# Kernel optimization log

Hardware: AMD Instinct MI355X
Metric: run time of the kernel (lower is better)

Reference implementation:

```python
import jax, jax.numpy as jnp
import numpy as np

B, D_IN, D_HID, D_OUT, E = 8192, 1024, 4096, 1024, 8


def setup_inputs() -> dict:
    key = jax.random.key(0)
    ks = jax.random.split(key, 6)
    s_in = 1.0 / np.sqrt(D_IN)
    s_gh = 1.0 / np.sqrt(D_HID // 2)
    s_eh = 1.0 / np.sqrt(D_HID)
    return {
        "x": jax.random.normal(ks[0], (B, D_IN), jnp.float32),
        "gW1": jax.random.normal(ks[1], (D_IN, D_HID // 2), jnp.float32) * s_in,
        "gb1": jnp.zeros((D_HID // 2,), jnp.float32),
        "gW2": jax.random.normal(ks[2], (D_HID // 2, E), jnp.float32) * s_gh,
        "gb2": jnp.zeros((E,), jnp.float32),
        "eW1": jax.random.normal(ks[3], (E, D_IN, D_HID), jnp.float32) * s_in,
        "eb1": jnp.zeros((E, D_HID), jnp.float32),
        "eW2": jax.random.normal(ks[4], (E, D_HID, D_OUT), jnp.float32) * s_eh,
        "eb2": jnp.zeros((E, D_OUT), jnp.float32),
    }


def reference(x, gW1, gb1, gW2, gb2, eW1, eb1, eW2, eb2):
    # Gating network: Linear -> ReLU -> (Dropout: eval identity) -> Linear -> Softmax(dim=1)
    gh = jax.nn.relu(x @ gW1 + gb1)                      # [B, H/2]
    gates = jax.nn.softmax(gh @ gW2 + gb2, axis=1)       # [B, E]

    # All experts run on the full batch (dense MoE): batched GEMMs over expert axis.
    h = jax.nn.relu(jnp.einsum('bi,eih->beh', x, eW1) + eb1)   # [B, E, H]
    eo = jnp.einsum('beh,eho->beo', h, eW2) + eb2              # [B, E, O]

    # Gated weighted sum over experts.
    combined = jnp.einsum('beo,be->bo', eo, gates)             # [B, O]
    return (combined, gates, gates)
```

## Files before the change

### kernel.cpp

```cpp
#include <hip/hip_runtime.h>
#include <hip/hip_bf16.h>
#include <stdint.h>

#define BB 8192
#define DIN 1024
#define DHID 4096
#define DOUT 1024
#define NEXP 8
#define GH_N 2048

typedef __attribute__((ext_vector_type(8))) __bf16 bf16x8;
typedef __attribute__((ext_vector_type(4))) float f32x4;

__device__ inline unsigned short f2bf(float f) {
  unsigned u = __builtin_bit_cast(unsigned, f);
  u = (u + 0x7FFFu + ((u >> 16) & 1u)) >> 16;
  return (unsigned short)u;
}
__device__ inline float b2f(unsigned short s) {
  return __builtin_bit_cast(float, (unsigned)s << 16);
}

__global__ void cvt_f32_bf16(const float* __restrict__ in,
                             unsigned short* __restrict__ out, int n4) {
  int i = blockIdx.x * blockDim.x + threadIdx.x;
  if (i >= n4) return;
  float4 v = ((const float4*)in)[i];
  ushort4 o;
  o.x = f2bf(v.x); o.y = f2bf(v.y); o.z = f2bf(v.z); o.w = f2bf(v.w);
  ((ushort4*)out)[i] = o;
}

__global__ void transpose_cvt(const float* __restrict__ in,
                              unsigned short* __restrict__ out, int R, int C) {
  __shared__ float tile[32][33];
  int c0 = blockIdx.x * 32, r0 = blockIdx.y * 32;
  int tx = threadIdx.x & 31, ty = threadIdx.x >> 5;
#pragma unroll
  for (int i = 0; i < 4; ++i)
    tile[ty + i * 8][tx] = in[(size_t)(r0 + ty + i * 8) * C + c0 + tx];
  __syncthreads();
#pragma unroll
  for (int i = 0; i < 4; ++i)
    out[(size_t)(c0 + ty + i * 8) * R + r0 + tx] = f2bf(tile[tx][ty + i * 8]);
}

__device__ inline void gload16(const void* g, void* l) {
  __builtin_amdgcn_global_load_lds(
      (const __attribute__((address_space(1))) void*)g,
      (__attribute__((address_space(3))) void*)l, 16, 0, 0);
}

template <int N>
__device__ inline void waitv() {
  if constexpr (N == 0) asm volatile("s_waitcnt vmcnt(0)" ::: "memory");
  else if constexpr (N == 2) asm volatile("s_waitcnt vmcnt(2)" ::: "memory");
  else asm volatile("s_waitcnt vmcnt(0)" ::: "memory");
}
__device__ inline void waitlgkm0() {
  asm volatile("s_waitcnt lgkmcnt(0)" ::: "memory");
  __builtin_amdgcn_sched_barrier(0);
}

template <int EPI>
__global__ __launch_bounds__(512, 4)
void gemmO(const unsigned short* __restrict__ A,
           const unsigned short* __restrict__ Bt,
           int M, int N, int K,
           const float* __restrict__ bias,
           unsigned short* __restrict__ outb,
           float* __restrict__ outf,
           const float* __restrict__ gates,
           int eidx, int accum) {
  constexpr int BK = 32;
  constexpr int TSZ = 128 * BK;
  __shared__ unsigned short As[3 * TSZ];
  __shared__ unsigned short Bs[3 * TSZ];

  const int t = threadIdx.x;
  const int lane = t & 63;
  const int wid = t >> 6;
  const int wm = wid >> 1;
  const int wn = wid & 1;

  const int nwg = gridDim.x;
  const int flat = blockIdx.x;
  const int swz = (flat & 7) * (nwg >> 3) + (flat >> 3);
  const int nbn = N >> 7;
  const int bn = swz % nbn, bm = swz / nbn;
  const int m0 = bm << 7, n0 = bn << 7;

  const int row = t >> 2, cp = t & 3;
  const int c = cp ^ ((row >> 1) & 3);
  const unsigned short* aS = A + (size_t)(m0 + row) * K + c * 8;
  const unsigned short* bS = Bt + (size_t)(n0 + row) * K + c * 8;
  const int qoff = t * 8;

  auto stage = [&](int T) {
    const int b = T % 3;
    const int k0 = T * BK;
    gload16(aS + k0, As + b * TSZ + qoff);
    gload16(bS + k0, Bs + b * TSZ + qoff);
  };

  const int l15 = lane & 15, lg = lane >> 4;
  int aoff[2], boff[4];
#pragma unroll
  for (int mi = 0; mi < 2; ++mi) {
    int r = wm * 32 + mi * 16 + l15;
    aoff[mi] = r * BK + ((lg ^ ((r >> 1) & 3)) << 3);
  }
#pragma unroll
  for (int ni = 0; ni < 4; ++ni) {
    int r = wn * 64 + ni * 16 + l15;
    boff[ni] = r * BK + ((lg ^ ((r >> 1) & 3)) << 3);
  }

  f32x4 acc[2][4];
  const f32x4 zero = {0.f, 0.f, 0.f, 0.f};
#pragma unroll
  for (int mi = 0; mi < 2; ++mi)
#pragma unroll
    for (int ni = 0; ni < 4; ++ni) acc[mi][ni] = zero;

  const int NT = K >> 5;

  stage(0);
  stage(1);
  waitv<2>();
  __builtin_amdgcn_s_barrier();

  for (int T = 0; T < NT; ++T) {
    const int b = T % 3;
    const unsigned short* Ab = As + b * TSZ;
    const unsigned short* Bb = Bs + b * TSZ;
    bf16x8 af[2], bfr[4];
#pragma unroll
    for (int mi = 0; mi < 2; ++mi) af[mi] = *(const bf16x8*)(Ab + aoff[mi]);
#pragma unroll
    for (int ni = 0; ni < 4; ++ni) bfr[ni] = *(const bf16x8*)(Bb + boff[ni]);
    if (T + 2 < NT) stage(T + 2);
    waitlgkm0();
    __builtin_amdgcn_s_setprio(1);
#pragma unroll
    for (int mi = 0; mi < 2; ++mi)
#pragma unroll
      for (int ni = 0; ni < 4; ++ni)
        acc[mi][ni] = __builtin_amdgcn_mfma_f32_16x16x32_bf16(
            af[mi], bfr[ni], acc[mi][ni], 0, 0, 0);
    __builtin_amdgcn_s_setprio(0);
    __builtin_amdgcn_sched_barrier(0);
    if (T + 2 < NT) waitv<2>();
    else if (T + 1 < NT) waitv<0>();
    __builtin_amdgcn_s_barrier();
  }

  const int rb = m0 + wm * 32 + (lg << 2);
  const int cb = n0 + wn * 64 + l15;
  if (EPI == 0) {
#pragma unroll
    for (int mi = 0; mi < 2; ++mi) {
#pragma unroll
      for (int ni = 0; ni < 4; ++ni) {
        int col = cb + ni * 16;
        float bv = bias[col];
#pragma unroll
        for (int r = 0; r < 4; ++r) {
          int rowo = rb + mi * 16 + r;
          float v = acc[mi][ni][r] + bv;
          outb[(size_t)rowo * N + col] = f2bf(fmaxf(v, 0.f));
        }
      }
    }
  } else {
#pragma unroll
    for (int mi = 0; mi < 2; ++mi) {
      float g[4];
#pragma unroll
      for (int r = 0; r < 4; ++r)
        g[r] = gates[(size_t)(rb + mi * 16 + r) * NEXP + eidx];
#pragma unroll
      for (int ni = 0; ni < 4; ++ni) {
        int col = cb + ni * 16;
        float bv = bias[col];
#pragma unroll
        for (int r = 0; r < 4; ++r) {
          size_t o = (size_t)(rb + mi * 16 + r) * N + col;
          float v = (acc[mi][ni][r] + bv) * g[r];
          outf[o] = accum ? outf[o] + v : v;
        }
      }
    }
  }
}

__global__ void gating_head(const unsigned short* __restrict__ gh,
                            const float* __restrict__ gW2,
                            const float* __restrict__ gb2,
                            float* __restrict__ gws,
                            float* __restrict__ g1,
                            float* __restrict__ g2, int B, int Kh) {
  int gw = (blockIdx.x * blockDim.x + threadIdx.x) >> 6;
  int lane = threadIdx.x & 63;
  int nw = (gridDim.x * blockDim.x) >> 6;
  for (int row = gw; row < B; row += nw) {
    float s[8] = {0, 0, 0, 0, 0, 0, 0, 0};
    for (int k = lane; k < Kh; k += 64) {
      float hv = b2f(gh[(size_t)row * Kh + k]);
      const float* w = gW2 + (size_t)k * 8;
#pragma unroll
      for (int e = 0; e < 8; ++e) s[e] += hv * w[e];
    }
#pragma unroll
    for (int e = 0; e < 8; ++e) {
#pragma unroll
      for (int off = 32; off > 0; off >>= 1) s[e] += __shfl_xor(s[e], off, 64);
    }
    if (lane == 0) {
      float l[8], m = -1e30f;
#pragma unroll
      for (int e = 0; e < 8; ++e) {
        l[e] = s[e] + gb2[e];
        m = fmaxf(m, l[e]);
      }
      float sum = 0.f;
#pragma unroll
      for (int e = 0; e < 8; ++e) {
        l[e] = expf(l[e] - m);
        sum += l[e];
      }
      float inv = 1.f / sum;
#pragma unroll
      for (int e = 0; e < 8; ++e) {
        float gv = l[e] * inv;
        gws[(size_t)row * 8 + e] = gv;
        g1[(size_t)row * 8 + e] = gv;
        g2[(size_t)row * 8 + e] = gv;
      }
    }
  }
}

extern "C" void kernel_launch(void* const* d_in, const int* in_sizes, int n_in,
                              void* d_out, int out_size, void* d_ws,
                              size_t ws_size, hipStream_t stream) {
  (void)in_sizes; (void)n_in; (void)out_size; (void)ws_size;
  const float* x   = (const float*)d_in[0];
  const float* gW1 = (const float*)d_in[1];
  const float* gb1 = (const float*)d_in[2];
  const float* gW2 = (const float*)d_in[3];
  const float* gb2 = (const float*)d_in[4];
  const float* eW1 = (const float*)d_in[5];
  const float* eb1 = (const float*)d_in[6];
  const float* eW2 = (const float*)d_in[7];
  const float* eb2 = (const float*)d_in[8];

  float* outC  = (float*)d_out;
  float* outG1 = outC + (size_t)BB * DOUT;
  float* outG2 = outG1 + (size_t)BB * NEXP;

  char* ws = (char*)d_ws;
  unsigned short* xb   = (unsigned short*)(ws);
  unsigned short* gW1T = (unsigned short*)(ws + 16777216);
  unsigned short* gh   = (unsigned short*)(ws + 20971520);
  float*          gat  = (float*)(ws + 54525952);
  unsigned short* w1T  = (unsigned short*)(ws + 54788096);
  unsigned short* w2T  = (unsigned short*)(ws + 63176704);
  unsigned short* hbuf = (unsigned short*)(ws + 71565312);

  cvt_f32_bf16<<<(BB * DIN / 4) / 256, 256, 0, stream>>>(x, xb, BB * DIN / 4);
  transpose_cvt<<<dim3(GH_N / 32, DIN / 32), 256, 0, stream>>>(gW1, gW1T, DIN, GH_N);
  gemmO<0><<<dim3((BB / 128) * (GH_N / 128)), 512, 0, stream>>>(
      xb, gW1T, BB, GH_N, DIN, gb1, gh, nullptr, nullptr, 0, 0);
  gating_head<<<256, 256, 0, stream>>>(gh, gW2, gb2, gat, outG1, outG2, BB, GH_N);

  for (int e = 0; e < NEXP; ++e) {
    transpose_cvt<<<dim3(DHID / 32, DIN / 32), 256, 0, stream>>>(
        eW1 + (size_t)e * DIN * DHID, w1T, DIN, DHID);
    transpose_cvt<<<dim3(DOUT / 32, DHID / 32), 256, 0, stream>>>(
        eW2 + (size_t)e * DHID * DOUT, w2T, DHID, DOUT);
    gemmO<0><<<dim3((BB / 128) * (DHID / 128)), 512, 0, stream>>>(
        xb, w1T, BB, DHID, DIN, eb1 + (size_t)e * DHID, hbuf, nullptr, nullptr, 0, 0);
    gemmO<1><<<dim3((BB / 128) * (DOUT / 128)), 512, 0, stream>>>(
        hbuf, w2T, BB, DOUT, DHID, eb2 + (size_t)e * DOUT, nullptr, outC, gat, e, e > 0);
  }
}
```

Before: 1.622 ms.

## Use larger 256-wide GEMM tiles with double-buffered quarter-phase pipeline; rewrite gating head

The 128x128 triple-buffered GEMM is replaced by a templated kernel using 256x256 tiles (or 128x256 for the second expert GEMM) with BK=64 and double buffering. Each K step is split into four MFMA phases, interleaving LDS fragment reads and async global-to-LDS loads between barriers. The aim is higher arithmetic intensity per LDS/global byte and better latency hiding, at the cost of fewer resident workgroups and many more barriers. The gating head is also rewritten to stage gW2 transposed in LDS, use vectorized loads, and assign one wave per row.

```diff
diff --git a/kernel.cpp b/kernel.cpp
--- a/kernel.cpp
+++ b/kernel.cpp
@@ -54,17 +54,21 @@
 template <int N>
 __device__ inline void waitv() {
   if constexpr (N == 0) asm volatile("s_waitcnt vmcnt(0)" ::: "memory");
+  else if constexpr (N == 1) asm volatile("s_waitcnt vmcnt(1)" ::: "memory");
   else if constexpr (N == 2) asm volatile("s_waitcnt vmcnt(2)" ::: "memory");
+  else if constexpr (N == 3) asm volatile("s_waitcnt vmcnt(3)" ::: "memory");
+  else if constexpr (N == 4) asm volatile("s_waitcnt vmcnt(4)" ::: "memory");
   else asm volatile("s_waitcnt vmcnt(0)" ::: "memory");
 }
 __device__ inline void waitlgkm0() {
   asm volatile("s_waitcnt lgkmcnt(0)" ::: "memory");
   __builtin_amdgcn_sched_barrier(0);
 }
-
-template <int EPI>
-__global__ __launch_bounds__(512, 4)
-void gemmO(const unsigned short* __restrict__ A,
+__device__ inline bf16x8 ldr(const char* p) { return *(const bf16x8*)p; }
+
+template <int BM, int EPI>
+__global__ __launch_bounds__(512, 2)
+void gemmP(const unsigned short* __restrict__ A,
            const unsigned short* __restrict__ Bt,
            int M, int N, int K,
            const float* __restrict__ bias,
@@ -72,121 +76,228 @@
            float* __restrict__ outf,
            const float* __restrict__ gates,
            int eidx, int accum) {
-  constexpr int BK = 32;
-  constexpr int TSZ = 128 * BK;
-  __shared__ unsigned short As[3 * TSZ];
-  __shared__ unsigned short Bs[3 * TSZ];
+  constexpr int BN = 256;
+  constexpr int WROWS = BM / 2;
+  constexpr int RM = WROWS / 16;
+  constexpr int HM = RM / 2;
+  constexpr int ABYTES = BM * 128;
+  constexpr int BBYTES = BN * 128;
+  constexpr int AUN = BM / 64;
+  constexpr int WS = (BM == 256) ? 4 : 3;
+  constexpr int W0L = (BM == 256) ? 2 : 1;
+
+  __shared__ char lds[2 * (ABYTES + BBYTES)];
+  char* Als = lds;
+  char* Bls = lds + 2 * ABYTES;
 
   const int t = threadIdx.x;
   const int lane = t & 63;
   const int wid = t >> 6;
-  const int wm = wid >> 1;
-  const int wn = wid & 1;
-
-  const int nwg = gridDim.x;
-  const int flat = blockIdx.x;
+  const int wm = wid >> 2;
+  const int wn = wid & 3;
+  const int l15 = lane & 15, lg = lane >> 4;
+
+  const int nwg = gridDim.x, flat = blockIdx.x;
   const int swz = (flat & 7) * (nwg >> 3) + (flat >> 3);
-  const int nbn = N >> 7;
+  const int nbn = N >> 8;
   const int bn = swz % nbn, bm = swz / nbn;
-  const int m0 = bm << 7, n0 = bn << 7;
-
-  const int row = t >> 2, cp = t & 3;
-  const int c = cp ^ ((row >> 1) & 3);
-  const unsigned short* aS = A + (size_t)(m0 + row) * K + c * 8;
-  const unsigned short* bS = Bt + (size_t)(n0 + row) * K + c * 8;
-  const int qoff = t * 8;
-
-  auto stage = [&](int T) {
-    const int b = T % 3;
-    const int k0 = T * BK;
-    gload16(aS + k0, As + b * TSZ + qoff);
-    gload16(bS + k0, Bs + b * TSZ + qoff);
-  };
-
-  const int l15 = lane & 15, lg = lane >> 4;
-  int aoff[2], boff[4];
-#pragma unroll
-  for (int mi = 0; mi < 2; ++mi) {
-    int r = wm * 32 + mi * 16 + l15;
-    aoff[mi] = r * BK + ((lg ^ ((r >> 1) & 3)) << 3);
-  }
-#pragma unroll
-  for (int ni = 0; ni < 4; ++ni) {
-    int r = wn * 64 + ni * 16 + l15;
-    boff[ni] = r * BK + ((lg ^ ((r >> 1) & 3)) << 3);
-  }
-
-  f32x4 acc[2][4];
+  const int m0 = bm * BM, n0 = bn * BN;
+
+  const int prow = t >> 3;
+  const int cOff = ((t & 7) ^ (prow & 7)) * 8;
+  const unsigned short* aP[AUN];
+  const unsigned short* bP[4];
+#pragma unroll
+  for (int u = 0; u < AUN; ++u) {
+    int p = u * 64 + prow;
+    int g;
+    if (BM == 256) g = ((p >> 6) & 1) * 128 + ((p >> 7) & 1) * 64 + (p & 63);
+    else           g = ((p >> 5) & 1) * 64  + ((p >> 6) & 1) * 32 + (p & 31);
+    aP[u] = A + (size_t)(m0 + g) * K + cOff;
+  }
+#pragma unroll
+  for (int u = 0; u < 4; ++u) {
+    int p = u * 64 + prow;
+    int g = ((p >> 5) & 3) * 64 + ((p >> 7) & 1) * 32 + (p & 31);
+    bP[u] = Bt + (size_t)(n0 + g) * K + cOff;
+  }
+  const int ldst = t * 16;
+
+  const int slot0 = ((lg) ^ (l15 & 7)) * 16;
+  const int slot1 = ((4 + lg) ^ (l15 & 7)) * 16;
+  const int aRB0 = (0 * (BM / 2) + wm * (WROWS / 2) + l15) * 128;
+  const int aRB1 = (1 * (BM / 2) + wm * (WROWS / 2) + l15) * 128;
+  const int bCB0 = (0 * (BN / 2) + wn * 32 + l15) * 128;
+  const int bCB1 = (1 * (BN / 2) + wn * 32 + l15) * 128;
+
+  f32x4 acc[RM][4];
   const f32x4 zero = {0.f, 0.f, 0.f, 0.f};
 #pragma unroll
-  for (int mi = 0; mi < 2; ++mi)
-#pragma unroll
-    for (int ni = 0; ni < 4; ++ni) acc[mi][ni] = zero;
-
-  const int NT = K >> 5;
-
-  stage(0);
-  stage(1);
-  waitv<2>();
+  for (int i = 0; i < RM; ++i)
+#pragma unroll
+    for (int j = 0; j < 4; ++j) acc[i][j] = zero;
+
+  bf16x8 ar[HM][2], bc0[2][2], bc1[2][2];
+
+  const int NT = K >> 6;
+
+  {
+    gload16(bP[0], Bls + 0 * 8192 + ldst);
+    gload16(bP[1], Bls + 1 * 8192 + ldst);
+    gload16(aP[0], Als + 0 * 8192 + ldst);
+    if (AUN == 4) gload16(aP[1], Als + 1 * 8192 + ldst);
+    gload16(bP[2], Bls + 2 * 8192 + ldst);
+    gload16(bP[3], Bls + 3 * 8192 + ldst);
+    if (AUN == 4) {
+      gload16(aP[2], Als + 2 * 8192 + ldst);
+      gload16(aP[3], Als + 3 * 8192 + ldst);
+    } else {
+      gload16(aP[1], Als + 1 * 8192 + ldst);
+    }
+  }
+  waitv<WS>();
   __builtin_amdgcn_s_barrier();
 
   for (int T = 0; T < NT; ++T) {
-    const int b = T % 3;
-    const unsigned short* Ab = As + b * TSZ;
-    const unsigned short* Bb = Bs + b * TSZ;
-    bf16x8 af[2], bfr[4];
-#pragma unroll
-    for (int mi = 0; mi < 2; ++mi) af[mi] = *(const bf16x8*)(Ab + aoff[mi]);
-#pragma unroll
-    for (int ni = 0; ni < 4; ++ni) bfr[ni] = *(const bf16x8*)(Bb + boff[ni]);
-    if (T + 2 < NT) stage(T + 2);
+    const int buf = T & 1;
+    const char* Ab = Als + buf * ABYTES;
+    const char* Bb = Bls + buf * BBYTES;
+    char* An = Als + (buf ^ 1) * ABYTES;
+    char* Bn = Bls + (buf ^ 1) * BBYTES;
+    const bool stg = (T + 1 < NT);
+    const int kn = (T + 1) << 6;
+
+#pragma unroll
+    for (int f = 0; f < HM; ++f) {
+      ar[f][0] = ldr(Ab + aRB0 + f * 2048 + slot0);
+      ar[f][1] = ldr(Ab + aRB0 + f * 2048 + slot1);
+    }
+#pragma unroll
+    for (int c = 0; c < 2; ++c) {
+      bc0[c][0] = ldr(Bb + bCB0 + c * 2048 + slot0);
+      bc0[c][1] = ldr(Bb + bCB0 + c * 2048 + slot1);
+    }
+    if (stg) {
+      gload16(bP[0] + kn, Bn + 0 * 8192 + ldst);
+      gload16(bP[1] + kn, Bn + 1 * 8192 + ldst);
+    }
+    __builtin_amdgcn_s_barrier();
     waitlgkm0();
     __builtin_amdgcn_s_setprio(1);
 #pragma unroll
-    for (int mi = 0; mi < 2; ++mi)
-#pragma unroll
-      for (int ni = 0; ni < 4; ++ni)
-        acc[mi][ni] = __builtin_amdgcn_mfma_f32_16x16x32_bf16(
-            af[mi], bfr[ni], acc[mi][ni], 0, 0, 0);
+    for (int ks = 0; ks < 2; ++ks)
+#pragma unroll
+      for (int f = 0; f < HM; ++f)
+#pragma unroll
+        for (int c = 0; c < 2; ++c)
+          acc[f][c] = __builtin_amdgcn_mfma_f32_16x16x32_bf16(
+              ar[f][ks], bc0[c][ks], acc[f][c], 0, 0, 0);
     __builtin_amdgcn_s_setprio(0);
-    __builtin_amdgcn_sched_barrier(0);
-    if (T + 2 < NT) waitv<2>();
-    else if (T + 1 < NT) waitv<0>();
-    __builtin_amdgcn_s_barrier();
-  }
-
-  const int rb = m0 + wm * 32 + (lg << 2);
+    if (stg) waitv<WS>(); else waitv<W0L>();
+    __builtin_amdgcn_s_barrier();
+
+#pragma unroll
+    for (int c = 0; c < 2; ++c) {
+      bc1[c][0] = ldr(Bb + bCB1 + c * 2048 + slot0);
+      bc1[c][1] = ldr(Bb + bCB1 + c * 2048 + slot1);
+    }
+    if (stg) {
+      gload16(aP[0] + kn, An + 0 * 8192 + ldst);
+      if (AUN == 4) gload16(aP[1] + kn, An + 1 * 8192 + ldst);
+    }
+    __builtin_amdgcn_s_barrier();
+    waitlgkm0();
+    __builtin_amdgcn_s_setprio(1);
+#pragma unroll
+    for (int ks = 0; ks < 2; ++ks)
+#pragma unroll
+      for (int f = 0; f < HM; ++f)
+#pragma unroll
+        for (int c = 0; c < 2; ++c)
+          acc[f][2 + c] = __builtin_amdgcn_mfma_f32_16x16x32_bf16(
+              ar[f][ks], bc1[c][ks], acc[f][2 + c], 0, 0, 0);
+    __builtin_amdgcn_s_setprio(0);
+    if (stg) waitv<WS>(); else waitv<0>();
+    __builtin_amdgcn_s_barrier();
+
+#pragma unroll
+    for (int f = 0; f < HM; ++f) {
+      ar[f][0] = ldr(Ab + aRB1 + f * 2048 + slot0);
+      ar[f][1] = ldr(Ab + aRB1 + f * 2048 + slot1);
+    }
+    if (stg) {
+      gload16(bP[2] + kn, Bn + 2 * 8192 + ldst);
+      gload16(bP[3] + kn, Bn + 3 * 8192 + ldst);
+    }
+    __builtin_amdgcn_s_barrier();
+    waitlgkm0();
+    __builtin_amdgcn_s_setprio(1);
+#pragma unroll
+    for (int ks = 0; ks < 2; ++ks)
+#pragma unroll
+      for (int f = 0; f < HM; ++f)
+#pragma unroll
+        for (int c = 0; c < 2; ++c)
+          acc[HM + f][2 + c] = __builtin_amdgcn_mfma_f32_16x16x32_bf16(
+              ar[f][ks], bc1[c][ks], acc[HM + f][2 + c], 0, 0, 0);
+    __builtin_amdgcn_s_setprio(0);
+    __builtin_amdgcn_s_barrier();
+
+    if (stg) {
+      if (AUN == 4) {
+        gload16(aP[2] + kn, An + 2 * 8192 + ldst);
+        gload16(aP[3] + kn, An + 3 * 8192 + ldst);
+      } else {
+        gload16(aP[1] + kn, An + 1 * 8192 + ldst);
+      }
+    }
+    __builtin_amdgcn_s_barrier();
+    __builtin_amdgcn_s_setprio(1);
+#pragma unroll
+    for (int ks = 0; ks < 2; ++ks)
+#pragma unroll
+      for (int f = 0; f < HM; ++f)
+#pragma unroll
+        for (int c = 0; c < 2; ++c)
+          acc[HM + f][c] = __builtin_amdgcn_mfma_f32_16x16x32_bf16(
+              ar[f][ks], bc0[c][ks], acc[HM + f][c], 0, 0, 0);
+    __builtin_amdgcn_s_setprio(0);
+    if (stg) waitv<WS>();
+    __builtin_amdgcn_s_barrier();
+  }
+
+  const int rb = m0 + wm * WROWS + (lg << 2);
   const int cb = n0 + wn * 64 + l15;
   if (EPI == 0) {
 #pragma unroll
-    for (int mi = 0; mi < 2; ++mi) {
-#pragma unroll
-      for (int ni = 0; ni < 4; ++ni) {
-        int col = cb + ni * 16;
+    for (int fg = 0; fg < RM; ++fg) {
+#pragma unroll
+      for (int j = 0; j < 4; ++j) {
+        int col = cb + j * 16;
         float bv = bias[col];
 #pragma unroll
         for (int r = 0; r < 4; ++r) {
-          int rowo = rb + mi * 16 + r;
-          float v = acc[mi][ni][r] + bv;
-          outb[(size_t)rowo * N + col] = f2bf(fmaxf(v, 0.f));
+          int row = rb + fg * 16 + r;
+          float v = acc[fg][j][r] + bv;
+          outb[(size_t)row * N + col] = f2bf(fmaxf(v, 0.f));
         }
       }
     }
   } else {
 #pragma unroll
-    for (int mi = 0; mi < 2; ++mi) {
+    for (int fg = 0; fg < RM; ++fg) {
       float g[4];
 #pragma unroll
       for (int r = 0; r < 4; ++r)
-        g[r] = gates[(size_t)(rb + mi * 16 + r) * NEXP + eidx];
-#pragma unroll
-      for (int ni = 0; ni < 4; ++ni) {
-        int col = cb + ni * 16;
+        g[r] = gates[(size_t)(rb + fg * 16 + r) * NEXP + eidx];
+#pragma unroll
+      for (int j = 0; j < 4; ++j) {
+        int col = cb + j * 16;
         float bv = bias[col];
 #pragma unroll
         for (int r = 0; r < 4; ++r) {
-          size_t o = (size_t)(rb + mi * 16 + r) * N + col;
-          float v = (acc[mi][ni][r] + bv) * g[r];
+          size_t o = (size_t)(rb + fg * 16 + r) * N + col;
+          float v = (acc[fg][j][r] + bv) * g[r];
           outf[o] = accum ? outf[o] + v : v;
         }
       }
@@ -194,49 +305,58 @@
   }
 }
 
-__global__ void gating_head(const unsigned short* __restrict__ gh,
-                            const float* __restrict__ gW2,
-                            const float* __restrict__ gb2,
-                            float* __restrict__ gws,
-                            float* __restrict__ g1,
-                            float* __restrict__ g2, int B, int Kh) {
-  int gw = (blockIdx.x * blockDim.x + threadIdx.x) >> 6;
-  int lane = threadIdx.x & 63;
-  int nw = (gridDim.x * blockDim.x) >> 6;
-  for (int row = gw; row < B; row += nw) {
-    float s[8] = {0, 0, 0, 0, 0, 0, 0, 0};
-    for (int k = lane; k < Kh; k += 64) {
-      float hv = b2f(gh[(size_t)row * Kh + k]);
-      const float* w = gW2 + (size_t)k * 8;
-#pragma unroll
-      for (int e = 0; e < 8; ++e) s[e] += hv * w[e];
-    }
+__global__ __launch_bounds__(512)
+void gating_head2(const unsigned short* __restrict__ gh,
+                  const float* __restrict__ gW2,
+                  const float* __restrict__ gb2,
+                  float* __restrict__ gws,
+                  float* __restrict__ g1,
+                  float* __restrict__ g2) {
+  __shared__ float wT[8][2048];
+  const int t = threadIdx.x;
+  for (int idx = t; idx < 16384; idx += 512) {
+    wT[idx & 7][idx >> 3] = gW2[idx];
+  }
+  __syncthreads();
+  const int wid = t >> 6, lane = t & 63;
+  const int row = blockIdx.x * 8 + wid;
+  const unsigned short* ghr = gh + (size_t)row * 2048;
+  float s[8] = {0.f, 0.f, 0.f, 0.f, 0.f, 0.f, 0.f, 0.f};
+#pragma unroll
+  for (int j = 0; j < 8; ++j) {
+    int k4 = lane + 64 * j;
+    ushort4 hv = ((const ushort4*)ghr)[k4];
+    float h0 = b2f(hv.x), h1 = b2f(hv.y), h2 = b2f(hv.z), h3 = b2f(hv.w);
 #pragma unroll
     for (int e = 0; e < 8; ++e) {
-#pragma unroll
-      for (int off = 32; off > 0; off >>= 1) s[e] += __shfl_xor(s[e], off, 64);
-    }
-    if (lane == 0) {
-      float l[8], m = -1e30f;
-#pragma unroll
-      for (int e = 0; e < 8; ++e) {
-        l[e] = s[e] + gb2[e];
-        m = fmaxf(m, l[e]);
-      }
-      float sum = 0.f;
-#pragma unroll
-      for (int e = 0; e < 8; ++e) {
-        l[e] = expf(l[e] - m);
-        sum += l[e];
-      }
-      float inv = 1.f / sum;
-#pragma unroll
-      for (int e = 0; e < 8; ++e) {
-        float gv = l[e] * inv;
-        gws[(size_t)row * 8 + e] = gv;
-        g1[(size_t)row * 8 + e] = gv;
-        g2[(size_t)row * 8 + e] = gv;
-      }
+      float4 w = ((const float4*)&wT[e][0])[k4];
+      s[e] += h0 * w.x + h1 * w.y + h2 * w.z + h3 * w.w;
+    }
+  }
+#pragma unroll
+  for (int e = 0; e < 8; ++e)
+#pragma unroll
+    for (int off = 1; off < 64; off <<= 1) s[e] += __shfl_xor(s[e], off, 64);
+  if (lane == 0) {
+    float l[8], m = -1e30f;
+#pragma unroll
+    for (int e = 0; e < 8; ++e) {
+      l[e] = s[e] + gb2[e];
+      m = fmaxf(m, l[e]);
+    }
+    float sum = 0.f;
+#pragma unroll
+    for (int e = 0; e < 8; ++e) {
+      l[e] = expf(l[e] - m);
+      sum += l[e];
+    }
+    float inv = 1.f / sum;
+#pragma unroll
+    for (int e = 0; e < 8; ++e) {
+      float gv = l[e] * inv;
+      gws[(size_t)row * 8 + e] = gv;
+      g1[(size_t)row * 8 + e] = gv;
+      g2[(size_t)row * 8 + e] = gv;
     }
   }
 }
@@ -270,18 +390,18 @@
 
   cvt_f32_bf16<<<(BB * DIN / 4) / 256, 256, 0, stream>>>(x, xb, BB * DIN / 4);
   transpose_cvt<<<dim3(GH_N / 32, DIN / 32), 256, 0, stream>>>(gW1, gW1T, DIN, GH_N);
-  gemmO<0><<<dim3((BB / 128) * (GH_N / 128)), 512, 0, stream>>>(
+  gemmP<256, 0><<<dim3((BB / 256) * (GH_N / 256)), 512, 0, stream>>>(
       xb, gW1T, BB, GH_N, DIN, gb1, gh, nullptr, nullptr, 0, 0);
-  gating_head<<<256, 256, 0, stream>>>(gh, gW2, gb2, gat, outG1, outG2, BB, GH_N);
+  gating_head2<<<BB / 8, 512, 0, stream>>>(gh, gW2, gb2, gat, outG1, outG2);
 
   for (int e = 0; e < NEXP; ++e) {
     transpose_cvt<<<dim3(DHID / 32, DIN / 32), 256, 0, stream>>>(
         eW1 + (size_t)e * DIN * DHID, w1T, DIN, DHID);
     transpose_cvt<<<dim3(DOUT / 32, DHID / 32), 256, 0, stream>>>(
         eW2 + (size_t)e * DHID * DOUT, w2T, DHID, DOUT);
-    gemmO<0><<<dim3((BB / 128) * (DHID / 128)), 512, 0, stream>>>(
+    gemmP<256, 0><<<dim3((BB / 256) * (DHID / 256)), 512, 0, stream>>>(
         xb, w1T, BB, DHID, DIN, eb1 + (size_t)e * DHID, hbuf, nullptr, nullptr, 0, 0);
-    gemmO<1><<<dim3((BB / 128) * (DOUT / 128)), 512, 0, stream>>>(
+    gemmP<128, 1><<<dim3((BB / 128) * (DOUT / 256)), 512, 0, stream>>>(
         hbuf, w2T, BB, DOUT, DHID, eb2 + (size_t)e * DOUT, nullptr, outC, gat, e, e > 0);
   }
 }
```

Result: faster. 1.416 ms (-12.7%).
